# Kernel tuning notes

Hardware: AMD Instinct MI355X
Metric: run time of the kernel (lower is better)

Reference implementation:

```python
import jax, jax.numpy as jnp
import numpy as np

B, S, E = 4, 2048, 1024
H, DK, DV = 16, 64, 128


def setup_inputs() -> dict:
    key = jax.random.key(0)
    ks = jax.random.split(key, 9)
    scale = 0.02
    x = jax.random.normal(ks[0], (B, S, E), dtype=jnp.float32)
    # Per-head linear weights stacked along a head axis (same math as the
    # torch ModuleList of nn.Linear(embed_dim, d) layers).
    Wq = jax.random.normal(ks[1], (H, E, DK), dtype=jnp.float32) * scale
    bq = jax.random.normal(ks[2], (H, DK), dtype=jnp.float32) * scale
    Wk = jax.random.normal(ks[3], (H, E, DK), dtype=jnp.float32) * scale
    bk = jax.random.normal(ks[4], (H, DK), dtype=jnp.float32) * scale
    Wv = jax.random.normal(ks[5], (H, E, DV), dtype=jnp.float32) * scale
    bv = jax.random.normal(ks[6], (H, DV), dtype=jnp.float32) * scale
    Wo = jax.random.normal(ks[7], (H * DV, E), dtype=jnp.float32) * scale
    bo = jax.random.normal(ks[8], (E,), dtype=jnp.float32) * scale
    return {"x": x, "Wq": Wq, "bq": bq, "Wk": Wk, "bk": bk,
            "Wv": Wv, "bv": bv, "Wo": Wo, "bo": bo}


def reference(x, Wq, bq, Wk, bk, Wv, bv, Wo, bo):
    # Batched equivalent of the per-head Linear loop: [B,S,E] x [H,E,D] -> [B,H,S,D]
    Q = jnp.einsum('bse,hed->bhsd', x, Wq) + bq[None, :, None, :]
    K = jnp.einsum('bse,hed->bhsd', x, Wk) + bk[None, :, None, :]
    V = jnp.einsum('bse,hed->bhsd', x, Wv) + bv[None, :, None, :]
    scale = 1.0 / jnp.sqrt(jnp.asarray(Q.shape[-1], dtype=Q.dtype))
    scores = jnp.einsum('bhqd,bhkd->bhqk', Q, K) * scale  # [B,H,S,S]
    causal_mask = jnp.triu(jnp.ones((S, S), dtype=bool), k=1)  # True above diagonal
    scores = jnp.where(causal_mask[None, None], jnp.asarray(-jnp.inf, scores.dtype), scores)
    probs = jax.nn.softmax(scores, axis=-1)
    attn = jnp.einsum('bhqk,bhkd->bhqd', probs, V)  # [B,H,S,DV]
    # transpose(1,2).view(B,S,H*DV)
    concat = attn.transpose(0, 2, 1, 3).reshape(x.shape[0], x.shape[1], -1)
    return concat @ Wo + bo
```

## Files before the change

kernel.cpp:

```cpp
#include <hip/hip_runtime.h>

typedef __bf16 bf16x8 __attribute__((ext_vector_type(8)));
typedef float f32x4 __attribute__((ext_vector_type(4)));
typedef float f32x16 __attribute__((ext_vector_type(16)));

static constexpr int Bb = 4, Ss = 2048, Ee = 1024, Hh = 16, DKk = 64, DVv = 128;
static constexpr int Mm = Bb * Ss;
static constexpr int NQ = Hh * DKk;
static constexpr int NV = Hh * DVv;

#define MFMA16 __builtin_amdgcn_mfma_f32_16x16x32_bf16
#define MFMA32 __builtin_amdgcn_mfma_f32_32x32x16_bf16

#define GLL16(g, l) __builtin_amdgcn_global_load_lds(                        \
    (const __attribute__((address_space(1))) void*)(g),                      \
    (__attribute__((address_space(3))) void*)(l), 16, 0, 0)

#define SBAR()   asm volatile("s_barrier" ::: "memory")
#define WLGKM0() do { asm volatile("s_waitcnt lgkmcnt(0)" ::: "memory"); \
                      __builtin_amdgcn_sched_barrier(0); } while (0)
#define WVM(n)   asm volatile("s_waitcnt vmcnt(" #n ")" ::: "memory")

static __device__ __forceinline__ unsigned short f2b(float f) {
  unsigned int u = __float_as_uint(f);
  u += 0x7fffu + ((u >> 16) & 1u);
  return (unsigned short)(u >> 16);
}

__global__ __launch_bounds__(256) void cast_x_kernel(const float* __restrict__ in,
                                                     unsigned short* __restrict__ out, int n4) {
  int i = blockIdx.x * 256 + threadIdx.x;
  if (i >= n4) return;
  float4 v = reinterpret_cast<const float4*>(in)[i];
  ushort4 o;
  o.x = f2b(v.x); o.y = f2b(v.y); o.z = f2b(v.z); o.w = f2b(v.w);
  reinterpret_cast<ushort4*>(out)[i] = o;
}

__global__ __launch_bounds__(256) void transpose_cast_kernel(const float* __restrict__ in,
                                                             unsigned short* __restrict__ out,
                                                             int R, int C) {
  __shared__ float tile[32][33];
  int c0 = blockIdx.x * 32, r0 = blockIdx.y * 32;
  const float* ip = in + (size_t)blockIdx.z * R * C;
  unsigned short* op = out + (size_t)blockIdx.z * R * C;
  int tx = threadIdx.x, ty = threadIdx.y;
#pragma unroll
  for (int i = 0; i < 32; i += 8)
    tile[ty + i][tx] = ip[(size_t)(r0 + ty + i) * C + (c0 + tx)];
  __syncthreads();
#pragma unroll
  for (int i = 0; i < 32; i += 8)
    op[(size_t)(c0 + ty + i) * R + (r0 + tx)] = f2b(tile[tx][ty + i]);
}

template <int OUTMODE>
__global__ __launch_bounds__(512, 2) void gemm8_kernel(const unsigned short* __restrict__ A,
                                                       const unsigned short* __restrict__ BT,
                                                       const float* __restrict__ bias1,
                                                       const float* __restrict__ bias2,
                                                       void* __restrict__ out1,
                                                       void* __restrict__ out2,
                                                       int N, int K) {
  __shared__ unsigned short As0[256 * 64], As1[256 * 64];
  __shared__ unsigned short Bs0[128 * 64], Bs1[128 * 64];
  const int tid = threadIdx.x, wave = tid >> 6, lane = tid & 63;
  const int wm = wave >> 1, wn = wave & 1;
  const int l15 = lane & 15, lq = lane >> 4;
  const int nwg = gridDim.x, cpx = nwg >> 3;
  const int orig = (blockIdx.x & 7) * cpx + (blockIdx.x >> 3);
  const int bm = (orig & 31) << 8, bn = (orig >> 5) << 7;
  const int srow = tid >> 3;
  const int ssw = (((tid & 7) ^ (srow & 7)) << 3);
  const int rsw = l15 & 7;
  const int nIter = K >> 7;

  f32x4 acc[4][4] = {};
  bf16x8 bf[2][4];

#define LDA(ASQ, MI, KK) \
  (*reinterpret_cast<const bf16x8*>(&(ASQ)[(size_t)((wm * 64 + (MI)*16 + l15) * 64) + (((((KK)*4 + lq)) ^ rsw) << 3)]))
#define LDB(BSQ, NI, KK) \
  (*reinterpret_cast<const bf16x8*>(&(BSQ)[(size_t)((wn * 64 + (NI)*16 + l15) * 64) + (((((KK)*4 + lq)) ^ rsw) << 3)]))

  auto stA = [&](unsigned short* dst, int kt) {
#pragma unroll
    for (int k4 = 0; k4 < 4; ++k4)
      GLL16(A + (size_t)(bm + srow + k4 * 64) * K + kt * 64 + ssw,
            &dst[(size_t)(tid + k4 * 512) * 8]);
  };
  auto stB = [&](unsigned short* dst, int kt) {
#pragma unroll
    for (int k4 = 0; k4 < 2; ++k4)
      GLL16(BT + (size_t)(bn + srow + k4 * 64) * K + kt * 64 + ssw,
            &dst[(size_t)(tid + k4 * 512) * 8]);
  };

  stA(As0, 0);
  stB(Bs0, 0);
  stB(Bs1, 1);
  WVM(0);
  SBAR();

  for (int it = 0; it < nIter; ++it) {
    const bool notlast = (it < nIter - 1);
    {
      bf16x8 af[2][2];
      af[0][0] = LDA(As0, 0, 0); af[0][1] = LDA(As0, 1, 0);
      af[1][0] = LDA(As0, 0, 1); af[1][1] = LDA(As0, 1, 1);
#pragma unroll
      for (int kk = 0; kk < 2; ++kk)
#pragma unroll
        for (int ni = 0; ni < 4; ++ni) bf[kk][ni] = LDB(Bs0, ni, kk);
      stA(As1, 2 * it + 1);
      SBAR();
      WLGKM0();
      __builtin_amdgcn_s_setprio(1);
#pragma unroll
      for (int kk = 0; kk < 2; ++kk)
#pragma unroll
        for (int i = 0; i < 2; ++i)
#pragma unroll
          for (int ni = 0; ni < 4; ++ni)
            acc[i][ni] = MFMA16(af[kk][i], bf[kk][ni], acc[i][ni], 0, 0, 0);
      __builtin_amdgcn_s_setprio(0);
      SBAR();
    }
    {
      bf16x8 af[2][2];
      af[0][0] = LDA(As0, 2, 0); af[0][1] = LDA(As0, 3, 0);
      af[1][0] = LDA(As0, 2, 1); af[1][1] = LDA(As0, 3, 1);
      if (notlast) stB(Bs0, 2 * it + 2);
      SBAR();
      WLGKM0();
      __builtin_amdgcn_s_setprio(1);
#pragma unroll
      for (int kk = 0; kk < 2; ++kk)
#pragma unroll
        for (int i = 0; i < 2; ++i)
#pragma unroll
          for (int ni = 0; ni < 4; ++ni)
            acc[2 + i][ni] = MFMA16(af[kk][i], bf[kk][ni], acc[2 + i][ni], 0, 0, 0);
      __builtin_amdgcn_s_setprio(0);
      if (notlast) { WVM(2); } else { WVM(0); }
      SBAR();
    }
    {
      bf16x8 af[2][2];
      af[0][0] = LDA(As1, 0, 0); af[0][1] = LDA(As1, 1, 0);
      af[1][0] = LDA(As1, 0, 1); af[1][1] = LDA(As1, 1, 1);
#pragma unroll
      for (int kk = 0; kk < 2; ++kk)
#pragma unroll
        for (int ni = 0; ni < 4; ++ni) bf[kk][ni] = LDB(Bs1, ni, kk);
      if (notlast) stA(As0, 2 * it + 2);
      SBAR();
      WLGKM0();
      __builtin_amdgcn_s_setprio(1);
#pragma unroll
      for (int kk = 0; kk < 2; ++kk)
#pragma unroll
        for (int i = 0; i < 2; ++i)
#pragma unroll
          for (int ni = 0; ni < 4; ++ni)
            acc[i][ni] = MFMA16(af[kk][i], bf[kk][ni], acc[i][ni], 0, 0, 0);
      __builtin_amdgcn_s_setprio(0);
      SBAR();
    }
    {
      bf16x8 af[2][2];
      af[0][0] = LDA(As1, 2, 0); af[0][1] = LDA(As1, 3, 0);
      af[1][0] = LDA(As1, 2, 1); af[1][1] = LDA(As1, 3, 1);
      if (notlast) stB(Bs1, 2 * it + 3);
      SBAR();
      WLGKM0();
      __builtin_amdgcn_s_setprio(1);
#pragma unroll
      for (int kk = 0; kk < 2; ++kk)
#pragma unroll
        for (int i = 0; i < 2; ++i)
#pragma unroll
          for (int ni = 0; ni < 4; ++ni)
            acc[2 + i][ni] = MFMA16(af[kk][i], bf[kk][ni], acc[2 + i][ni], 0, 0, 0);
      __builtin_amdgcn_s_setprio(0);
      if (notlast) WVM(2);
      SBAR();
    }
  }

  const float SCLQ = 0.125f * 1.44269504088896f;
#pragma unroll
  for (int ni = 0; ni < 4; ++ni) {
    int col = bn + wn * 64 + ni * 16 + l15;
    float bs;
    if (OUTMODE == 4)
      bs = (col < 1024) ? bias1[col] : bias2[col - 1024];
    else
      bs = bias1[col];
#pragma unroll
    for (int mi = 0; mi < 4; ++mi) {
      int row0 = bm + wm * 64 + mi * 16 + (lq << 2);
      if (OUTMODE == 2) {
        int b_ = row0 >> 11, s0 = row0 & 2047;
        unsigned short* dst = (unsigned short*)out1 +
            ((size_t)((b_ * Hh + (col >> 7)) * DVv + (col & 127))) * Ss + s0;
        ushort4 o;
        o.x = f2b(acc[mi][ni][0] + bs);
        o.y = f2b(acc[mi][ni][1] + bs);
        o.z = f2b(acc[mi][ni][2] + bs);
        o.w = f2b(acc[mi][ni][3] + bs);
        *reinterpret_cast<ushort4*>(dst) = o;
      } else if (OUTMODE == 4) {
        unsigned short* tgt = (unsigned short*)(col < 1024 ? out1 : out2);
        int cc = col & 1023, hh = cc >> 6, d = cc & 63;
#pragma unroll
        for (int r = 0; r < 4; ++r) {
          int row = row0 + r;
          int b_ = row >> 11, s0 = row & 2047;
          float v = acc[mi][ni][r] + bs;
          if (col < 1024) v *= SCLQ;
          tgt[(((size_t)(b_ * Hh + hh) * Ss + s0) << 6) + d] = f2b(v);
        }
      } else {
#pragma unroll
        for (int r = 0; r < 4; ++r)
          reinterpret_cast<float*>(out1)[(size_t)(row0 + r) * N + col] = acc[mi][ni][r] + bs;
      }
    }
  }
#undef LDA
#undef LDB
}

__global__ __launch_bounds__(512, 1) void attn11_kernel(const unsigned short* __restrict__ Qh,
                                                        const unsigned short* __restrict__ Kh,
                                                        const unsigned short* __restrict__ Vt,
                                                        unsigned short* __restrict__ Aw) {
  __shared__ unsigned short Kb[2][64 * 64];
  __shared__ unsigned short Vb[2][128 * 64];
  const int bid = blockIdx.x;
  const int phase = bid >> 8, idx = bid & 255;
  const int xcd = idx & 7, sub = idx >> 3;
  const int bhL = sub >> 2, q = sub & 3;
  const int bh = xcd + (bhL << 3);
  const int b = bh >> 4, h = bh & 15;
  const int qt = phase ? q : 7 - q;
  const int tid = threadIdx.x, wave = tid >> 6, lane = tid & 63;
  const int l31 = lane & 31, lh = lane >> 5;

  const unsigned short* Qsrc = Qh + (size_t)(b * Hh + h) * Ss * DKk;
  const unsigned short* Ksrc = Kh + (size_t)(b * Hh + h) * Ss * DKk;
  const unsigned short* Vsrc = Vt + (size_t)(b * Hh + h) * (size_t)DVv * Ss;
  unsigned short* Adst = Aw + (size_t)b * Ss * NV + h * DVv;

  const int nt = (qt + 1) * 4;
  const int q0w = qt * 256 + wave * 32;

  const int srow = tid >> 3, sch = tid & 7;
  const int soff = ((sch ^ (srow & 7)) << 3);
  const int rx = l31 & 7;

  union PU { unsigned u[4]; bf16x8 v; };

  bf16x8 qf[4];
#pragma unroll
  for (int ks = 0; ks < 4; ++ks)
    qf[ks] = *reinterpret_cast<const bf16x8*>(
        Qsrc + (size_t)(q0w + l31) * DKk + ks * 16 + lh * 8);

  f32x16 accO[4] = {};
  float mrow = -1e30f, lrow = 0.f;

  {
    GLL16(Ksrc + (size_t)srow * DKk + soff, &Kb[0][(size_t)tid * 8]);
    GLL16(Vsrc + (size_t)srow * Ss + soff, &Vb[0][(size_t)tid * 8]);
    GLL16(Vsrc + (size_t)(srow + 64) * Ss + soff, &Vb[0][(size_t)(tid + 512) * 8]);
  }

  for (int kt = 0; kt < nt; ++kt) {
    const int kbase = kt * 64;
    const int cur = kt & 1;
    __syncthreads();
    if (kt + 1 < nt) {
      const int nb = kbase + 64;
      const int nxt = cur ^ 1;
      GLL16(Ksrc + (size_t)(nb + srow) * DKk + soff, &Kb[nxt][(size_t)tid * 8]);
      GLL16(Vsrc + (size_t)srow * Ss + nb + soff, &Vb[nxt][(size_t)tid * 8]);
      GLL16(Vsrc + (size_t)(srow + 64) * Ss + nb + soff, &Vb[nxt][(size_t)(tid + 512) * 8]);
    }
    if (kbase > q0w + 31) continue;

    f32x16 accS[2] = {};
    __builtin_amdgcn_s_setprio(1);
#pragma unroll
    for (int kvb = 0; kvb < 2; ++kvb)
#pragma unroll
      for (int ks = 0; ks < 4; ++ks) {
        const unsigned short* kr = &Kb[cur][(kvb * 32 + l31) * 64];
        bf16x8 kf = *reinterpret_cast<const bf16x8*>(kr + (((ks * 2 + lh) ^ rx) << 3));
        accS[kvb] = MFMA32(kf, qf[ks], accS[kvb], 0, 0, 0);
      }
    __builtin_amdgcn_s_setprio(0);

    if (kbase + 63 > q0w) {
      int qg = q0w + l31;
#pragma unroll
      for (int kvb = 0; kvb < 2; ++kvb)
#pragma unroll
        for (int reg = 0; reg < 16; ++reg) {
          int kvg = kbase + kvb * 32 + (reg & 3) + 8 * (reg >> 2) + 4 * lh;
          if (kvg > qg) accS[kvb][reg] = -1e30f;
        }
    }
    float t[8];
#pragma unroll
    for (int i = 0; i < 8; ++i)
      t[i] = fmaxf(fmaxf(accS[0][i], accS[0][i + 8]), fmaxf(accS[1][i], accS[1][i + 8]));
    float pmx = fmaxf(fmaxf(fmaxf(t[0], t[1]), fmaxf(t[2], t[3])),
                      fmaxf(fmaxf(t[4], t[5]), fmaxf(t[6], t[7])));
    pmx = fmaxf(pmx, __shfl_xor(pmx, 32));
    float mn = mrow;
    if (!__all(pmx - mn <= 8.f)) {
      float mnew = fmaxf(mn, pmx);
      float al = exp2f(mn - mnew);
      mrow = mnew;
      lrow *= al;
#pragma unroll
      for (int reg = 0; reg < 16; ++reg) {
        float a = __shfl(al, (reg & 3) + 8 * (reg >> 2) + 4 * lh);
#pragma unroll
        for (int dvb = 0; dvb < 4; ++dvb) accO[dvb][reg] *= a;
      }
      mn = mnew;
    }
    float rs = 0.f;
#pragma unroll
    for (int kvb = 0; kvb < 2; ++kvb)
#pragma unroll
      for (int reg = 0; reg < 16; ++reg) {
        float e = exp2f(accS[kvb][reg] - mn);
        accS[kvb][reg] = e;
        rs += e;
      }
    rs += __shfl_xor(rs, 32);
    lrow += rs;
    bf16x8 pfrag[4];
#pragma unroll
    for (int kvb = 0; kvb < 2; ++kvb)
#pragma unroll
      for (int s = 0; s < 2; ++s) {
        const int B0 = s * 8;
        unsigned a, c, bb, d;
        asm("v_cvt_pk_bf16_f32 %0, %1, %2" : "=v"(a) : "v"(accS[kvb][B0 + 0]), "v"(accS[kvb][B0 + 1]));
        asm("v_cvt_pk_bf16_f32 %0, %1, %2" : "=v"(c) : "v"(accS[kvb][B0 + 2]), "v"(accS[kvb][B0 + 3]));
        asm("v_cvt_pk_bf16_f32 %0, %1, %2" : "=v"(bb) : "v"(accS[kvb][B0 + 4]), "v"(accS[kvb][B0 + 5]));
        asm("v_cvt_pk_bf16_f32 %0, %1, %2" : "=v"(d) : "v"(accS[kvb][B0 + 6]), "v"(accS[kvb][B0 + 7]));
        asm volatile("v_permlane32_swap_b32 %0, %1" : "+v"(a), "+v"(bb));
        asm volatile("v_permlane32_swap_b32 %0, %1" : "+v"(c), "+v"(d));
        PU u;
        u.u[0] = a; u.u[1] = c; u.u[2] = bb; u.u[3] = d;
        pfrag[kvb * 2 + s] = u.v;
      }
    __builtin_amdgcn_s_setprio(1);
#pragma unroll
    for (int dvb = 0; dvb < 4; ++dvb) {
      const unsigned short* vr = &Vb[cur][(dvb * 32 + l31) * 64];
#pragma unroll
      for (int ks = 0; ks < 4; ++ks) {
        bf16x8 vf = *reinterpret_cast<const bf16x8*>(vr + (((ks * 2 + lh) ^ rx) << 3));
        accO[dvb] = MFMA32(pfrag[ks], vf, accO[dvb], 0, 0, 0);
      }
    }
    __builtin_amdgcn_s_setprio(0);
  }
  float linv = 1.f / lrow;
#pragma unroll
  for (int reg = 0; reg < 16; ++reg) {
    int qr = (reg & 3) + 8 * (reg >> 2) + 4 * lh;
    float li = __shfl(linv, qr);
    int row = q0w + qr;
#pragma unroll
    for (int dvb = 0; dvb < 4; ++dvb)
      Adst[(size_t)row * NV + dvb * 32 + l31] = f2b(accO[dvb][reg] * li);
  }
}

extern "C" void kernel_launch(void* const* d_in, const int* in_sizes, int n_in,
                              void* d_out, int out_size, void* d_ws, size_t ws_size,
                              hipStream_t stream) {
  (void)in_sizes; (void)n_in; (void)out_size; (void)ws_size;
  const float* x  = (const float*)d_in[0];
  const float* Wq = (const float*)d_in[1];
  const float* bq = (const float*)d_in[2];
  const float* Wk = (const float*)d_in[3];
  const float* bk = (const float*)d_in[4];
  const float* Wv = (const float*)d_in[5];
  const float* bv = (const float*)d_in[6];
  const float* Wo = (const float*)d_in[7];
  const float* bo = (const float*)d_in[8];
  float* out = (float*)d_out;

  unsigned short* ws = (unsigned short*)d_ws;
  unsigned short* xb  = ws;
  unsigned short* WqT = xb  + 8388608;
  unsigned short* WkT = WqT + 1048576;
  unsigned short* WvT = WkT + 1048576;
  unsigned short* WoT = WvT + 2097152;
  unsigned short* Qw  = WoT + 2097152;
  unsigned short* Kw  = Qw  + 8388608;
  unsigned short* Vtw = Kw  + 8388608;
  unsigned short* Aw  = Vtw + 16777216;

  cast_x_kernel<<<dim3(8192), dim3(256), 0, stream>>>(x, xb, (Mm * Ee) / 4);

  transpose_cast_kernel<<<dim3(2, 32, 16), dim3(32, 8), 0, stream>>>(Wq, WqT, Ee, DKk);
  transpose_cast_kernel<<<dim3(2, 32, 16), dim3(32, 8), 0, stream>>>(Wk, WkT, Ee, DKk);
  transpose_cast_kernel<<<dim3(4, 32, 16), dim3(32, 8), 0, stream>>>(Wv, WvT, Ee, DVv);
  transpose_cast_kernel<<<dim3(32, 64, 1), dim3(32, 8), 0, stream>>>(Wo, WoT, NV, Ee);

  gemm8_kernel<4><<<dim3(512), dim3(512), 0, stream>>>(xb, WqT, bq, bk, Qw, Kw, 2048, Ee);
  gemm8_kernel<2><<<dim3(512), dim3(512), 0, stream>>>(xb, WvT, bv, nullptr, Vtw, nullptr, NV, Ee);

  attn11_kernel<<<dim3(512), dim3(512), 0, stream>>>(Qw, Kw, Vtw, Aw);

  gemm8_kernel<1><<<dim3(256), dim3(512), 0, stream>>>(Aw, WoT, bo, nullptr, out, nullptr, NQ, NV);
}
```

Before: 306.3 us.

## Use 256x256 output tiles for QKV projection GEMMs with 8 waves in 2x4 layout

Adds a gemm9 kernel whose block computes a 256x256 tile instead of 256x128, with waves arranged 2x4 and each wave holding 8x4 accumulator fragments. The Q/K and V projections launch half as many blocks. The goal is higher arithmetic intensity and less global/LDS traffic per MFMA. The output-projection GEMM moves to a separate fp32-output specialization. In exchange, LDS use doubles to 128KB per block and accumulator registers double, so occupancy likely falls to one block per CU. The 256-block grid may also underfill the GPU.

Result: faster. 282.4 us (-7.8%).

```diff
diff --git a/kernel.cpp b/kernel.cpp
--- a/kernel.cpp
+++ b/kernel.cpp
@@ -55,13 +55,192 @@
 }
 
 template <int OUTMODE>
-__global__ __launch_bounds__(512, 2) void gemm8_kernel(const unsigned short* __restrict__ A,
+__global__ __launch_bounds__(512, 2) void gemm9_kernel(const unsigned short* __restrict__ A,
                                                        const unsigned short* __restrict__ BT,
                                                        const float* __restrict__ bias1,
                                                        const float* __restrict__ bias2,
                                                        void* __restrict__ out1,
                                                        void* __restrict__ out2,
                                                        int N, int K) {
+  __shared__ unsigned short As0[256 * 64], As1[256 * 64];
+  __shared__ unsigned short Bs0[256 * 64], Bs1[256 * 64];
+  const int tid = threadIdx.x, wave = tid >> 6, lane = tid & 63;
+  const int wm = wave >> 2, wn = wave & 3;
+  const int l15 = lane & 15, lq = lane >> 4;
+  const int nwg = gridDim.x, cpx = nwg >> 3;
+  const int orig = (blockIdx.x & 7) * cpx + (blockIdx.x >> 3);
+  const int bm = (orig & 31) << 8, bn = (orig >> 5) << 8;
+  const int srow = tid >> 3;
+  const int ssw = (((tid & 7) ^ (srow & 7)) << 3);
+  const int rsw = l15 & 7;
+  const int nIter = K >> 7;
+
+  f32x4 acc[8][4] = {};
+  bf16x8 bf[2][4];
+
+#define LDA9(ASQ, MI, KK) \
+  (*reinterpret_cast<const bf16x8*>(&(ASQ)[(size_t)((wm * 128 + (MI)*16 + l15) * 64) + (((((KK)*4 + lq)) ^ rsw) << 3)]))
+#define LDB9(BSQ, NI, KK) \
+  (*reinterpret_cast<const bf16x8*>(&(BSQ)[(size_t)((wn * 64 + (NI)*16 + l15) * 64) + (((((KK)*4 + lq)) ^ rsw) << 3)]))
+
+  auto stA = [&](unsigned short* dst, int kt) {
+#pragma unroll
+    for (int k4 = 0; k4 < 4; ++k4)
+      GLL16(A + (size_t)(bm + srow + k4 * 64) * K + kt * 64 + ssw,
+            &dst[(size_t)(tid + k4 * 512) * 8]);
+  };
+  auto stB = [&](unsigned short* dst, int kt) {
+#pragma unroll
+    for (int k4 = 0; k4 < 4; ++k4)
+      GLL16(BT + (size_t)(bn + srow + k4 * 64) * K + kt * 64 + ssw,
+            &dst[(size_t)(tid + k4 * 512) * 8]);
+  };
+
+  stA(As0, 0);
+  stB(Bs0, 0);
+  stB(Bs1, 1);
+  WVM(0);
+  SBAR();
+
+  for (int it = 0; it < nIter; ++it) {
+    const bool notlast = (it < nIter - 1);
+    {
+      bf16x8 af[2][4];
+#pragma unroll
+      for (int kk = 0; kk < 2; ++kk)
+#pragma unroll
+        for (int m = 0; m < 4; ++m) af[kk][m] = LDA9(As0, m, kk);
+#pragma unroll
+      for (int kk = 0; kk < 2; ++kk)
+#pragma unroll
+        for (int ni = 0; ni < 4; ++ni) bf[kk][ni] = LDB9(Bs0, ni, kk);
+      stA(As1, 2 * it + 1);
+      SBAR();
+      WLGKM0();
+      __builtin_amdgcn_s_setprio(1);
+#pragma unroll
+      for (int kk = 0; kk < 2; ++kk)
+#pragma unroll
+        for (int m = 0; m < 4; ++m)
+#pragma unroll
+          for (int ni = 0; ni < 4; ++ni)
+            acc[m][ni] = MFMA16(af[kk][m], bf[kk][ni], acc[m][ni], 0, 0, 0);
+      __builtin_amdgcn_s_setprio(0);
+      SBAR();
+    }
+    {
+      bf16x8 af[2][4];
+#pragma unroll
+      for (int kk = 0; kk < 2; ++kk)
+#pragma unroll
+        for (int m = 0; m < 4; ++m) af[kk][m] = LDA9(As0, 4 + m, kk);
+      if (notlast) stB(Bs0, 2 * it + 2);
+      SBAR();
+      WLGKM0();
+      __builtin_amdgcn_s_setprio(1);
+#pragma unroll
+      for (int kk = 0; kk < 2; ++kk)
+#pragma unroll
+        for (int m = 0; m < 4; ++m)
+#pragma unroll
+          for (int ni = 0; ni < 4; ++ni)
+            acc[4 + m][ni] = MFMA16(af[kk][m], bf[kk][ni], acc[4 + m][ni], 0, 0, 0);
+      __builtin_amdgcn_s_setprio(0);
+      if (notlast) { WVM(4); } else { WVM(0); }
+      SBAR();
+    }
+    {
+      bf16x8 af[2][4];
+#pragma unroll
+      for (int kk = 0; kk < 2; ++kk)
+#pragma unroll
+        for (int m = 0; m < 4; ++m) af[kk][m] = LDA9(As1, m, kk);
+#pragma unroll
+      for (int kk = 0; kk < 2; ++kk)
+#pragma unroll
+        for (int ni = 0; ni < 4; ++ni) bf[kk][ni] = LDB9(Bs1, ni, kk);
+      if (notlast) stA(As0, 2 * it + 2);
+      SBAR();
+      WLGKM0();
+      __builtin_amdgcn_s_setprio(1);
+#pragma unroll
+      for (int kk = 0; kk < 2; ++kk)
+#pragma unroll
+        for (int m = 0; m < 4; ++m)
+#pragma unroll
+          for (int ni = 0; ni < 4; ++ni)
+            acc[m][ni] = MFMA16(af[kk][m], bf[kk][ni], acc[m][ni], 0, 0, 0);
+      __builtin_amdgcn_s_setprio(0);
+      SBAR();
+    }
+    {
+      bf16x8 af[2][4];
+#pragma unroll
+      for (int kk = 0; kk < 2; ++kk)
+#pragma unroll
+        for (int m = 0; m < 4; ++m) af[kk][m] = LDA9(As1, 4 + m, kk);
+      if (notlast) stB(Bs1, 2 * it + 3);
+      SBAR();
+      WLGKM0();
+      __builtin_amdgcn_s_setprio(1);
+#pragma unroll
+      for (int kk = 0; kk < 2; ++kk)
+#pragma unroll
+        for (int m = 0; m < 4; ++m)
+#pragma unroll
+          for (int ni = 0; ni < 4; ++ni)
+            acc[4 + m][ni] = MFMA16(af[kk][m], bf[kk][ni], acc[4 + m][ni], 0, 0, 0);
+      __builtin_amdgcn_s_setprio(0);
+      if (notlast) WVM(4);
+      SBAR();
+    }
+  }
+
+  const float SCLQ = 0.125f * 1.44269504088896f;
+#pragma unroll
+  for (int ni = 0; ni < 4; ++ni) {
+    int col = bn + wn * 64 + ni * 16 + l15;
+    float bs;
+    if (OUTMODE == 4)
+      bs = (col < 1024) ? bias1[col] : bias2[col - 1024];
+    else
+      bs = bias1[col];
+#pragma unroll
+    for (int mi = 0; mi < 8; ++mi) {
+      int row0 = bm + wm * 128 + mi * 16 + (lq << 2);
+      if (OUTMODE == 2) {
+        int b_ = row0 >> 11, s0 = row0 & 2047;
+        unsigned short* dst = (unsigned short*)out1 +
+            ((size_t)((b_ * Hh + (col >> 7)) * DVv + (col & 127))) * Ss + s0;
+        ushort4 o;
+        o.x = f2b(acc[mi][ni][0] + bs);
+        o.y = f2b(acc[mi][ni][1] + bs);
+        o.z = f2b(acc[mi][ni][2] + bs);
+        o.w = f2b(acc[mi][ni][3] + bs);
+        *reinterpret_cast<ushort4*>(dst) = o;
+      } else {
+        unsigned short* tgt = (unsigned short*)(col < 1024 ? out1 : out2);
+        int cc = col & 1023, hh = cc >> 6, d = cc & 63;
+#pragma unroll
+        for (int r = 0; r < 4; ++r) {
+          int row = row0 + r;
+          int b_ = row >> 11, s0 = row & 2047;
+          float v = acc[mi][ni][r] + bs;
+          if (col < 1024) v *= SCLQ;
+          tgt[(((size_t)(b_ * Hh + hh) * Ss + s0) << 6) + d] = f2b(v);
+        }
+      }
+    }
+  }
+#undef LDA9
+#undef LDB9
+}
+
+__global__ __launch_bounds__(512, 2) void gemm8f_kernel(const unsigned short* __restrict__ A,
+                                                        const unsigned short* __restrict__ BT,
+                                                        const float* __restrict__ bias1,
+                                                        float* __restrict__ out1,
+                                                        int N, int K) {
   __shared__ unsigned short As0[256 * 64], As1[256 * 64];
   __shared__ unsigned short Bs0[128 * 64], Bs1[128 * 64];
   const int tid = threadIdx.x, wave = tid >> 6, lane = tid & 63;
@@ -188,44 +367,16 @@
     }
   }
 
-  const float SCLQ = 0.125f * 1.44269504088896f;
 #pragma unroll
   for (int ni = 0; ni < 4; ++ni) {
     int col = bn + wn * 64 + ni * 16 + l15;
-    float bs;
-    if (OUTMODE == 4)
-      bs = (col < 1024) ? bias1[col] : bias2[col - 1024];
-    else
-      bs = bias1[col];
+    float bs = bias1[col];
 #pragma unroll
     for (int mi = 0; mi < 4; ++mi) {
       int row0 = bm + wm * 64 + mi * 16 + (lq << 2);
-      if (OUTMODE == 2) {
-        int b_ = row0 >> 11, s0 = row0 & 2047;
-        unsigned short* dst = (unsigned short*)out1 +
-            ((size_t)((b_ * Hh + (col >> 7)) * DVv + (col & 127))) * Ss + s0;
-        ushort4 o;
-        o.x = f2b(acc[mi][ni][0] + bs);
-        o.y = f2b(acc[mi][ni][1] + bs);
-        o.z = f2b(acc[mi][ni][2] + bs);
-        o.w = f2b(acc[mi][ni][3] + bs);
-        *reinterpret_cast<ushort4*>(dst) = o;
-      } else if (OUTMODE == 4) {
-        unsigned short* tgt = (unsigned short*)(col < 1024 ? out1 : out2);
-        int cc = col & 1023, hh = cc >> 6, d = cc & 63;
-#pragma unroll
-        for (int r = 0; r < 4; ++r) {
-          int row = row0 + r;
-          int b_ = row >> 11, s0 = row & 2047;
-          float v = acc[mi][ni][r] + bs;
-          if (col < 1024) v *= SCLQ;
-          tgt[(((size_t)(b_ * Hh + hh) * Ss + s0) << 6) + d] = f2b(v);
-        }
-      } else {
-#pragma unroll
-        for (int r = 0; r < 4; ++r)
-          reinterpret_cast<float*>(out1)[(size_t)(row0 + r) * N + col] = acc[mi][ni][r] + bs;
-      }
+#pragma unroll
+      for (int r = 0; r < 4; ++r)
+        out1[(size_t)(row0 + r) * N + col] = acc[mi][ni][r] + bs;
     }
   }
 #undef LDA
@@ -418,10 +569,10 @@
   transpose_cast_kernel<<<dim3(4, 32, 16), dim3(32, 8), 0, stream>>>(Wv, WvT, Ee, DVv);
   transpose_cast_kernel<<<dim3(32, 64, 1), dim3(32, 8), 0, stream>>>(Wo, WoT, NV, Ee);
 
-  gemm8_kernel<4><<<dim3(512), dim3(512), 0, stream>>>(xb, WqT, bq, bk, Qw, Kw, 2048, Ee);
-  gemm8_kernel<2><<<dim3(512), dim3(512), 0, stream>>>(xb, WvT, bv, nullptr, Vtw, nullptr, NV, Ee);
+  gemm9_kernel<4><<<dim3(256), dim3(512), 0, stream>>>(xb, WqT, bq, bk, Qw, Kw, 2048, Ee);
+  gemm9_kernel<2><<<dim3(256), dim3(512), 0, stream>>>(xb, WvT, bv, nullptr, Vtw, nullptr, NV, Ee);
 
   attn11_kernel<<<dim3(512), dim3(512), 0, stream>>>(Qw, Kw, Vtw, Aw);
 
-  gemm8_kernel<1><<<dim3(256), dim3(512), 0, stream>>>(Aw, WoT, bo, nullptr, out, nullptr, NQ, NV);
-}
+  gemm8f_kernel<<<dim3(256), dim3(512), 0, stream>>>(Aw, WoT, bo, out, NQ, NV);
+}
```
